# Kernel tuning notes

Measured on AMD Instinct MI355X. Metric: run time of the kernel, lower is better.

The kernel has to match this reference:

```python
import jax, jax.numpy as jnp
import numpy as np

B, D = 4096, 256
TEMP = 0.5
EPS = 1e-8  # torch CosineSimilarity eps


def setup_inputs() -> dict:
    key = jax.random.key(0)
    k1, k2 = jax.random.split(key)
    return {
        "proj1": jax.random.normal(k1, (B, D), dtype=jnp.float32),
        "proj2": jax.random.normal(k2, (B, D), dtype=jnp.float32),
    }


def reference(proj1, proj2):
    b = proj1.shape[0]
    n = 2 * b
    z = jnp.concatenate([proj1, proj2], axis=0)  # [2B, D]
    # cosine similarity with clamped norms (matches torch.nn.CosineSimilarity)
    norm = jnp.maximum(jnp.linalg.norm(z, axis=1, keepdims=True), EPS)
    zn = z / norm
    sim = (zn @ zn.T) / TEMP  # [2B, 2B]
    # positives: diag(sim, +B) and diag(sim, -B)
    pos = jnp.concatenate([jnp.diagonal(sim, b), jnp.diagonal(sim, -b)])  # [2B]
    # CE with label 0 over logits [pos, negatives]. The negatives exclude the
    # diagonal and the positive pair, but the positive is re-included as
    # logits[:, 0], so the logsumexp runs over all entries except the diagonal.
    diag_mask = jnp.eye(n, dtype=bool)
    lse = jax.nn.logsumexp(jnp.where(diag_mask, -jnp.inf, sim), axis=1)  # [2B]
    loss = jnp.sum(lse - pos) / n
    return loss
```

## Files before the change

### kernel.cpp

```cpp
#include <hip/hip_runtime.h>
#include <hip/hip_bf16.h>

#define N_TOT 8192
#define B_HALF 4096
#define D_DIM 256
#define NQUAD 496
#define NSING 96
#define NBLK (NQUAD + NSING)
#define NREP 8

typedef __attribute__((ext_vector_type(4))) float f32x4;
typedef unsigned long long u64;

#define S8SCALE 27.178307f
#define LN2 0.69314718056f

__global__ __launch_bounds__(256) void k_norm(const float* __restrict__ p1,
                                              const float* __restrict__ p2,
                                              u64* __restrict__ zt,
                                              float* __restrict__ self,
                                              float* __restrict__ partials,
                                              float* __restrict__ RS,
                                              float* __restrict__ out) {
  __shared__ unsigned sm[2][8][64];
  __shared__ float red[4];
  int tid = threadIdx.x;
  int lane = tid & 63;
  int w = tid >> 6;
  int bid = blockIdx.x;
  int i0 = bid * 8;
  if (tid < 32) reinterpret_cast<f32x4*>(RS)[bid * 32 + tid] = (f32x4){0.f, 0.f, 0.f, 0.f};
  if (bid == 0 && tid == 0) out[0] = 0.0f;

  float possum = 0.f;
#pragma unroll
  for (int k = 0; k < 2; ++k) {
    int r = w * 2 + k;
    int i = i0 + r;
    float4 a = *reinterpret_cast<const float4*>(p1 + (size_t)i * D_DIM + lane * 4);
    float4 b = *reinterpret_cast<const float4*>(p2 + (size_t)i * D_DIM + lane * 4);
    float ssa = a.x * a.x + a.y * a.y + a.z * a.z + a.w * a.w;
    float ssb = b.x * b.x + b.y * b.y + b.z * b.z + b.w * b.w;
    float d = a.x * b.x + a.y * b.y + a.z * b.z + a.w * b.w;
#pragma unroll
    for (int m = 1; m < 64; m <<= 1) {
      ssa += __shfl_xor(ssa, m, 64);
      ssb += __shfl_xor(ssb, m, 64);
      d += __shfl_xor(d, m, 64);
    }
    float na = fmaxf(sqrtf(ssa), 1e-8f);
    float nb = fmaxf(sqrtf(ssb), 1e-8f);
    float ia = S8SCALE / na, ib = S8SCALE / nb;

    int wa = __builtin_amdgcn_cvt_pk_fp8_f32(a.x * ia, a.y * ia, 0, false);
    wa = __builtin_amdgcn_cvt_pk_fp8_f32(a.z * ia, a.w * ia, wa, true);
    int wb = __builtin_amdgcn_cvt_pk_fp8_f32(b.x * ib, b.y * ib, 0, false);
    wb = __builtin_amdgcn_cvt_pk_fp8_f32(b.z * ib, b.w * ib, wb, true);
    sm[0][r][lane] = (unsigned)wa;
    sm[1][r][lane] = (unsigned)wb;

    float va0 = __builtin_amdgcn_cvt_f32_fp8(wa, 0);
    float va1 = __builtin_amdgcn_cvt_f32_fp8(wa, 1);
    float va2 = __builtin_amdgcn_cvt_f32_fp8(wa, 2);
    float va3 = __builtin_amdgcn_cvt_f32_fp8(wa, 3);
    float vb0 = __builtin_amdgcn_cvt_f32_fp8(wb, 0);
    float vb1 = __builtin_amdgcn_cvt_f32_fp8(wb, 1);
    float vb2 = __builtin_amdgcn_cvt_f32_fp8(wb, 2);
    float vb3 = __builtin_amdgcn_cvt_f32_fp8(wb, 3);
    float sqa = va0 * va0 + va1 * va1 + va2 * va2 + va3 * va3;
    float sqb = vb0 * vb0 + vb1 * vb1 + vb2 * vb2 + vb3 * vb3;
#pragma unroll
    for (int m = 1; m < 64; m <<= 1) {
      sqa += __shfl_xor(sqa, m, 64);
      sqb += __shfl_xor(sqb, m, 64);
    }
    if (lane == 0) {
      self[i] = sqa * (1.0f / 256.0f);
      self[i + B_HALF] = sqb * (1.0f / 256.0f);
      possum += -4.0f * d / (na * nb) * (1.0f / (float)N_TOT);
    }
  }
  if (lane == 0) red[w] = possum;
  __syncthreads();
  if (tid == 0) partials[bid] = red[0] + red[1] + red[2] + red[3];

  {
    int h = tid >> 7;
    int rem = tid & 127;
    int g = rem >> 2;
    int qr = rem & 3;
    uint4 v;
    v.x = sm[h][qr * 2][g * 2];
    v.y = sm[h][qr * 2][g * 2 + 1];
    v.z = sm[h][qr * 2 + 1][g * 2];
    v.w = sm[h][qr * 2 + 1][g * 2 + 1];
    size_t idx8 = (size_t)g * N_TOT + h * B_HALF + i0 + qr * 2;
    *reinterpret_cast<uint4*>((char*)zt + idx8 * 8) = v;
  }
}

__global__ __launch_bounds__(256, 1) void k_sim(const u64* __restrict__ zt,
                                                float* __restrict__ RS) {
  const int bid = blockIdx.x;
  int ti = 0, cum = 0, tj0, nt;
  if (bid < NQUAD) {
    while (cum + ((64 - ti) >> 2) <= bid) { cum += (64 - ti) >> 2; ++ti; }
    tj0 = ti + 4 * (bid - cum);
    nt = 4;
  } else {
    const int s = bid - NQUAD;
    while (cum + ((64 - ti) & 3) <= s) { cum += (64 - ti) & 3; ++ti; }
    tj0 = 64 - ((64 - ti) & 3) + (s - cum);
    nt = 1;
  }
  const int nht = 2 * nt;
  const bool diag = (tj0 == ti);
  const int rowbase = ti * 128;
  const int colchunk = tj0 * 128;
  float* __restrict__ rowsum = RS + (size_t)(bid & (NREP - 1)) * N_TOT;

  const int tid = threadIdx.x;
  const int lane = tid & 63;
  const int wid = tid >> 6;
  const int wm = wid >> 1;
  const int wn = wid & 1;
  const int hi = lane >> 4;
  const int lo = lane & 15;

  const size_t baseA = (size_t)hi * N_TOT + rowbase + wm * 64 + lo;
  const size_t baseB = (size_t)hi * N_TOT + colchunk + wn * 32 + lo;

  long af[4][8];
#pragma unroll
  for (int m = 0; m < 4; ++m)
#pragma unroll
    for (int g = 0; g < 8; ++g)
      af[m][g] = (long)zt[(size_t)g * 4 * N_TOT + baseA + m * 16];

  float pr[4][4] = {};
  long bf[2][8];
  float fl0 = 0.f, fl1 = 0.f;
  int colPrev = 0;

#pragma unroll 1
  for (int t = 0; t < nht; ++t) {
    const int colT = colchunk + t * 64 + wn * 32;
#pragma unroll
    for (int nb = 0; nb < 2; ++nb)
#pragma unroll
      for (int g = 0; g < 8; ++g)
        bf[nb][g] = (long)zt[(size_t)g * 4 * N_TOT + baseB + t * 64 + nb * 16];
    __builtin_amdgcn_sched_barrier(0);
    if (t > 0 && hi == 0) {
      atomicAdd(&rowsum[colPrev + lo], fl0);
      atomicAdd(&rowsum[colPrev + 16 + lo], fl1);
    }
    __builtin_amdgcn_sched_barrier(0);
    if (t == 0) {
      asm volatile("s_waitcnt vmcnt(0)" ::: "memory");
    } else {
      asm volatile("s_waitcnt vmcnt(2)" ::: "memory");
    }
    __builtin_amdgcn_sched_barrier(0);

    f32x4 acc[4][2];
#pragma unroll
    for (int m = 0; m < 4; ++m)
#pragma unroll
      for (int n = 0; n < 2; ++n) acc[m][n] = (f32x4){0.f, 0.f, 0.f, 0.f};
#pragma unroll
    for (int g = 0; g < 8; ++g) {
      acc[0][0] = __builtin_amdgcn_mfma_f32_16x16x32_fp8_fp8(af[0][g], bf[0][g], acc[0][0], 0, 0, 0);
      acc[0][1] = __builtin_amdgcn_mfma_f32_16x16x32_fp8_fp8(af[0][g], bf[1][g], acc[0][1], 0, 0, 0);
      acc[1][0] = __builtin_amdgcn_mfma_f32_16x16x32_fp8_fp8(af[1][g], bf[0][g], acc[1][0], 0, 0, 0);
      acc[1][1] = __builtin_amdgcn_mfma_f32_16x16x32_fp8_fp8(af[1][g], bf[1][g], acc[1][1], 0, 0, 0);
      acc[2][0] = __builtin_amdgcn_mfma_f32_16x16x32_fp8_fp8(af[2][g], bf[0][g], acc[2][0], 0, 0, 0);
      acc[2][1] = __builtin_amdgcn_mfma_f32_16x16x32_fp8_fp8(af[2][g], bf[1][g], acc[2][1], 0, 0, 0);
      acc[3][0] = __builtin_amdgcn_mfma_f32_16x16x32_fp8_fp8(af[3][g], bf[0][g], acc[3][0], 0, 0, 0);
      acc[3][1] = __builtin_amdgcn_mfma_f32_16x16x32_fp8_fp8(af[3][g], bf[1][g], acc[3][1], 0, 0, 0);
    }

    float pc[2] = {0.f, 0.f};
#pragma unroll
    for (int m = 0; m < 4; ++m)
#pragma unroll
      for (int n = 0; n < 2; ++n) {
        float e0 = __builtin_amdgcn_exp2f(acc[m][n][0] * (1.0f / 256.0f));
        float e1 = __builtin_amdgcn_exp2f(acc[m][n][1] * (1.0f / 256.0f));
        float e2 = __builtin_amdgcn_exp2f(acc[m][n][2] * (1.0f / 256.0f));
        float e3 = __builtin_amdgcn_exp2f(acc[m][n][3] * (1.0f / 256.0f));
        pr[m][0] += e0; pr[m][1] += e1; pr[m][2] += e2; pr[m][3] += e3;
        pc[n] += (e0 + e1) + (e2 + e3);
      }
    float v0 = pc[0];
    v0 += __shfl_xor(v0, 16, 64);
    v0 += __shfl_xor(v0, 32, 64);
    float v1 = pc[1];
    v1 += __shfl_xor(v1, 16, 64);
    v1 += __shfl_xor(v1, 32, 64);
    const bool skip = (diag && t < 2);
    fl0 = skip ? 0.f : v0;
    fl1 = skip ? 0.f : v1;
    colPrev = colT;
  }
  if (hi == 0) {
    atomicAdd(&rowsum[colPrev + lo], fl0);
    atomicAdd(&rowsum[colPrev + 16 + lo], fl1);
  }

#pragma unroll
  for (int m = 0; m < 4; ++m)
#pragma unroll
    for (int r = 0; r < 4; ++r) {
      float s = pr[m][r];
      s += __shfl_xor(s, 1, 64);
      s += __shfl_xor(s, 2, 64);
      s += __shfl_xor(s, 4, 64);
      s += __shfl_xor(s, 8, 64);
      if (lo == 0)
        atomicAdd(&rowsum[rowbase + wm * 64 + m * 16 + hi * 4 + r], s);
    }
}

__global__ __launch_bounds__(256) void k_lse(const float* __restrict__ RS,
                                             const float* __restrict__ self,
                                             const float* __restrict__ partials,
                                             float* __restrict__ out) {
  int tid = threadIdx.x;
  int i = blockIdx.x * 256 + tid;
  float rs = 0.f;
#pragma unroll
  for (int r = 0; r < NREP; ++r) rs += RS[(size_t)r * N_TOT + i];
  rs -= __builtin_amdgcn_exp2f(self[i]);
  float v = __builtin_amdgcn_logf(rs) * (LN2 / (float)N_TOT);
  if (tid < 16) v += partials[blockIdx.x * 16 + tid];
#pragma unroll
  for (int m = 1; m < 64; m <<= 1) v += __shfl_xor(v, m, 64);
  __shared__ float red[4];
  if ((tid & 63) == 0) red[tid >> 6] = v;
  __syncthreads();
  if (tid == 0) atomicAdd(out, red[0] + red[1] + red[2] + red[3]);
}

extern "C" void kernel_launch(void* const* d_in, const int* in_sizes, int n_in,
                              void* d_out, int out_size, void* d_ws, size_t ws_size,
                              hipStream_t stream) {
  const float* p1 = (const float*)d_in[0];
  const float* p2 = (const float*)d_in[1];
  float* out = (float*)d_out;
  char* ws = (char*)d_ws;

  u64* zt = (u64*)ws;
  float* self = (float*)(ws + 2097152);
  float* RS = self + N_TOT;
  float* partials = RS + (size_t)NREP * N_TOT;

  k_norm<<<N_TOT / 16, 256, 0, stream>>>(p1, p2, zt, self, partials, RS, out);
  k_sim<<<NBLK, 256, 0, stream>>>(zt, RS);
  k_lse<<<N_TOT / 256, 256, 0, stream>>>(RS, self, partials, out);
}
```

Measured before the change: 34.07 us.

## Stage A tile in LDS and raise occupancy of fp8 similarity kernel

Moves the 128-row A operand from per-thread registers into a padded shared-memory tile and reads it from LDS inside the MFMA loop. Launch bounds change from 1 to 4 blocks per CU so more waves can be resident. This frees many VGPRs to allow higher occupancy and latency hiding. The cost is LDS reads on every tile iteration, a block-wide barrier, and possible bank conflicts on the 64-bit padded layout.

```diff
diff --git a/kernel.cpp b/kernel.cpp
--- a/kernel.cpp
+++ b/kernel.cpp
@@ -99,8 +99,10 @@
   }
 }
 
-__global__ __launch_bounds__(256, 1) void k_sim(const u64* __restrict__ zt,
+__global__ __launch_bounds__(256, 4) void k_sim(const u64* __restrict__ zt,
                                                 float* __restrict__ RS) {
+  __shared__ u64 A_s[128 * 33];
+
   const int bid = blockIdx.x;
   int ti = 0, cum = 0, tj0, nt;
   if (bid < NQUAD) {
@@ -127,15 +129,17 @@
   const int hi = lane >> 4;
   const int lo = lane & 15;
 
-  const size_t baseA = (size_t)hi * N_TOT + rowbase + wm * 64 + lo;
+#pragma unroll
+  for (int i = 0; i < 16; ++i) {
+    int q = i * 256 + tid;
+    int c = q >> 7;
+    int row = q & 127;
+    A_s[row * 33 + c] = zt[(size_t)c * N_TOT + rowbase + row];
+  }
+  __syncthreads();
+
   const size_t baseB = (size_t)hi * N_TOT + colchunk + wn * 32 + lo;
-
-  long af[4][8];
-#pragma unroll
-  for (int m = 0; m < 4; ++m)
-#pragma unroll
-    for (int g = 0; g < 8; ++g)
-      af[m][g] = (long)zt[(size_t)g * 4 * N_TOT + baseA + m * 16];
+  const int arow = wm * 64 + lo;
 
   float pr[4][4] = {};
   long bf[2][8];
@@ -170,14 +174,19 @@
       for (int n = 0; n < 2; ++n) acc[m][n] = (f32x4){0.f, 0.f, 0.f, 0.f};
 #pragma unroll
     for (int g = 0; g < 8; ++g) {
-      acc[0][0] = __builtin_amdgcn_mfma_f32_16x16x32_fp8_fp8(af[0][g], bf[0][g], acc[0][0], 0, 0, 0);
-      acc[0][1] = __builtin_amdgcn_mfma_f32_16x16x32_fp8_fp8(af[0][g], bf[1][g], acc[0][1], 0, 0, 0);
-      acc[1][0] = __builtin_amdgcn_mfma_f32_16x16x32_fp8_fp8(af[1][g], bf[0][g], acc[1][0], 0, 0, 0);
-      acc[1][1] = __builtin_amdgcn_mfma_f32_16x16x32_fp8_fp8(af[1][g], bf[1][g], acc[1][1], 0, 0, 0);
-      acc[2][0] = __builtin_amdgcn_mfma_f32_16x16x32_fp8_fp8(af[2][g], bf[0][g], acc[2][0], 0, 0, 0);
-      acc[2][1] = __builtin_amdgcn_mfma_f32_16x16x32_fp8_fp8(af[2][g], bf[1][g], acc[2][1], 0, 0, 0);
-      acc[3][0] = __builtin_amdgcn_mfma_f32_16x16x32_fp8_fp8(af[3][g], bf[0][g], acc[3][0], 0, 0, 0);
-      acc[3][1] = __builtin_amdgcn_mfma_f32_16x16x32_fp8_fp8(af[3][g], bf[1][g], acc[3][1], 0, 0, 0);
+      const int c8 = g * 4 + hi;
+      long a0 = (long)A_s[(size_t)(arow)*33 + c8];
+      long a1 = (long)A_s[(size_t)(arow + 16) * 33 + c8];
+      long a2 = (long)A_s[(size_t)(arow + 32) * 33 + c8];
+      long a3 = (long)A_s[(size_t)(arow + 48) * 33 + c8];
+      acc[0][0] = __builtin_amdgcn_mfma_f32_16x16x32_fp8_fp8(a0, bf[0][g], acc[0][0], 0, 0, 0);
+      acc[0][1] = __builtin_amdgcn_mfma_f32_16x16x32_fp8_fp8(a0, bf[1][g], acc[0][1], 0, 0, 0);
+      acc[1][0] = __builtin_amdgcn_mfma_f32_16x16x32_fp8_fp8(a1, bf[0][g], acc[1][0], 0, 0, 0);
+      acc[1][1] = __builtin_amdgcn_mfma_f32_16x16x32_fp8_fp8(a1, bf[1][g], acc[1][1], 0, 0, 0);
+      acc[2][0] = __builtin_amdgcn_mfma_f32_16x16x32_fp8_fp8(a2, bf[0][g], acc[2][0], 0, 0, 0);
+      acc[2][1] = __builtin_amdgcn_mfma_f32_16x16x32_fp8_fp8(a2, bf[1][g], acc[2][1], 0, 0, 0);
+      acc[3][0] = __builtin_amdgcn_mfma_f32_16x16x32_fp8_fp8(a3, bf[0][g], acc[3][0], 0, 0, 0);
+      acc[3][1] = __builtin_amdgcn_mfma_f32_16x16x32_fp8_fp8(a3, bf[1][g], acc[3][1], 0, 0, 0);
     }
 
     float pc[2] = {0.f, 0.f};
```

Result: no change. 34.06 us (-0.0%).
